# Kernel optimization log

Measured on AMD Instinct MI355X. Metric: run time of the kernel, lower is better.

The kernel has to match this reference:

```python
import jax, jax.numpy as jnp
import numpy as np

F_NHID = 64
C_NHID = 64
U_INIT = F_NHID + C_NHID + 1   # 129
U_OUT = F_NHID + C_NHID        # 128
U_HID = 128
N_AGG = 4
M_INIT = 3 * N_AGG * U_OUT + C_NHID  # 1600
M_HID = 256
M_OUT = C_NHID


def setup_inputs() -> dict:
    key = jax.random.key(0)
    ks = jax.random.split(key, 12)
    B, Nc, Nf = 4, 512, 256
    h_fac = jax.random.normal(ks[0], (B, Nf, F_NHID), dtype=jnp.float32)
    h_cus = jax.random.normal(ks[1], (B, Nc, C_NHID), dtype=jnp.float32)
    edge = jax.random.normal(ks[2], (B, Nc, Nf, 1), dtype=jnp.float32)
    adj = jax.random.randint(ks[3], (B, Nc, Nf), 0, 2).astype(jnp.float32)
    def lin(k, i, o):
        return jax.random.normal(k, (i, o), dtype=jnp.float32) / np.sqrt(i)
    return {
        'h_fac': h_fac, 'h_cus': h_cus, 'edge': edge, 'adj': adj,
        'U_W1': lin(ks[4], U_INIT, U_HID), 'U_b1': jnp.zeros((U_HID,), jnp.float32),
        'U_W2': lin(ks[5], U_HID, U_OUT), 'U_b2': jnp.zeros((U_OUT,), jnp.float32),
        'M_W1': lin(ks[6], M_INIT, M_HID), 'M_b1': jnp.zeros((M_HID,), jnp.float32),
        'M_W2': lin(ks[7], M_HID, M_OUT), 'M_b2': jnp.zeros((M_OUT,), jnp.float32),
    }


def reference(h_fac, h_cus, edge, adj, U_W1, U_b1, U_W2, U_b2, M_W1, M_b1, M_W2, M_b2):
    B, Nc, c = h_cus.shape
    Nf = h_fac.shape[1]
    # Per-edge message input: [customer_feat, facility_feat, edge_scalar] -> (B,Nc,Nf,U_INIT)
    msg = jnp.concatenate([
        jnp.broadcast_to(h_cus[:, :, None, :], (B, Nc, Nf, c)),
        jnp.broadcast_to(h_fac[:, None, :, :], (B, Nc, Nf, h_fac.shape[-1])),
        edge,
    ], axis=-1)
    # U MLP (pretransformation): relu -> linear
    m = jax.nn.relu(msg @ U_W1 + U_b1)
    m = m @ U_W2 + U_b2  # (B, Nc, Nf, U_OUT)

    mask = adj > 0                              # (B, Nc, Nf)
    maskf = mask[..., None].astype(m.dtype)     # (B, Nc, Nf, 1)
    cnt = jnp.sum(maskf, axis=2)                # (B, Nc, 1)
    mean = jnp.sum(m * maskf, axis=2) / cnt     # nanmean over masked entries
    var = jnp.sum(((m - mean[:, :, None, :]) ** 2) * maskf, axis=2) / cnt
    std = jnp.sqrt(var)                         # population std (divides by count)
    mx = jnp.max(jnp.where(mask[..., None], m, -jnp.inf), axis=2)
    mn = jnp.min(jnp.where(mask[..., None], m, jnp.inf), axis=2)

    # Degree-based scalers (get_avgd + scale_amplification/attenuation)
    deg_c = jnp.sum(adj, axis=-1)               # (B, Nc)
    deg_f = jnp.sum(adj, axis=-2)               # (B, Nf)
    avg_d = jnp.mean(jnp.concatenate([jnp.log(deg_c + 1.0), jnp.log(deg_f + 1.0)], axis=-1), axis=-1)  # (B,)
    scale = (jnp.log(deg_c + 1.0) / avg_d[:, None])[..., None]          # (B, Nc, 1)
    scale_inv = jnp.where(scale != 0, 1.0 / scale, jnp.zeros_like(scale))

    feats = [h_cus]
    for a in (mean, std, mx, mn):
        feats.extend([a, a * scale, a * scale_inv])
    h = jnp.concatenate(feats, axis=-1)         # (B, Nc, M_INIT)

    # M MLP (posttransformation): relu -> linear (last activation 'none')
    h = jax.nn.relu(h @ M_W1 + M_b1)
    out = h @ M_W2 + M_b2                       # (B, Nc, C_NHID)
    return out
```

## Files before the change

kernel.cpp:

```cpp
#include <hip/hip_runtime.h>
#include <hip/hip_bf16.h>


using bs8 = __attribute__((ext_vector_type(8))) short;
using f4  = __attribute__((ext_vector_type(4))) float;

__device__ __forceinline__ unsigned short f2bf(float f) {
    union { float f; unsigned int u; } x; x.f = f;
    unsigned int u = x.u + 0x7FFFu + ((x.u >> 16) & 1u);
    return (unsigned short)(u >> 16);
}

__device__ __forceinline__ unsigned int pkbf(float a, float b) {
    __hip_bfloat162 h = __float22bfloat162_rn(make_float2(a, b));
    union { __hip_bfloat162 h; unsigned int u; } c; c.h = h;
    return c.u;
}

__global__ void PNALayer_35081292874189_kernel() {}

#define OFF_AC     0u
#define OFF_AF     1048576u
#define OFF_DEGC   1572864u
#define OFF_DEGF   1581056u
#define OFF_SCALE  1585152u
#define OFF_SINV   1593344u
#define OFF_FEATB  1601536u
#define OFF_HMID   8155392u
#define OFF_W2T    10252544u
#define OFF_W1TB   10318080u
#define WS_NEED    11170048u

__global__ void PNALayer_ws_fail(float* out, int n) {
    int i = blockIdx.x * 256 + threadIdx.x;
    if (i < n) out[i] = 2500.0f;
}

__global__ void PNALayer_prep1(
    const float* h_fac, const float* h_cus, const float* adj,
    const float* U_W1, const float* U_b1, const float* U_W2, const float* M_W1,
    float* wsAc, float* wsAf, float* wsDegC, float* wsDegF,
    unsigned short* wsW2Tb, unsigned short* wsW1Tb)
{
    __shared__ float sH[64];
    __shared__ float sRed[256];
    __shared__ float sT[64][65];
    int bid = blockIdx.x, t = threadIdx.x;

    if (bid < 1024) {
        int b = bid >> 8, f = bid & 255;
        if (t < 64) sH[t] = h_fac[(b * 256 + f) * 64 + t];
        __syncthreads();
        if (t < 128) {
            float acc = 0.f;
            for (int k = 0; k < 64; ++k)
                acc += sH[k] * U_W1[(64 + k) * 128 + t];
            wsAf[(b * 256 + f) * 128 + t] = acc;
        }
        float v = adj[(b * 512 + t) * 256 + f] + adj[(b * 512 + t + 256) * 256 + f];
        sRed[t] = v; __syncthreads();
        for (int s = 128; s > 0; s >>= 1) { if (t < s) sRed[t] += sRed[t + s]; __syncthreads(); }
        if (t == 0) wsDegF[b * 256 + f] = sRed[0];
    } else if (bid < 3072) {
        int bc = bid - 1024;
        if (t < 64) sH[t] = h_cus[bc * 64 + t];
        __syncthreads();
        if (t < 128) {
            float acc = U_b1[t];
            for (int k = 0; k < 64; ++k)
                acc += sH[k] * U_W1[k * 128 + t];
            wsAc[bc * 128 + t] = acc;
        }
        float v = adj[bc * 256 + t];
        sRed[t] = v; __syncthreads();
        for (int s = 128; s > 0; s >>= 1) { if (t < s) sRed[t] += sRed[t + s]; __syncthreads(); }
        if (t == 0) wsDegC[bc] = sRed[0];
    } else if (bid < 3076) {
        int l = bid - 3072;
        int k0 = (l >> 1) * 64, n0 = (l & 1) * 64;
        for (int rep = 0; rep < 16; ++rep) {
            int idx = rep * 256 + t; int r = idx >> 6, c = idx & 63;
            sT[r][c] = U_W2[(k0 + r) * 128 + n0 + c];
        }
        __syncthreads();
        for (int rep = 0; rep < 16; ++rep) {
            int idx = rep * 256 + t; int r = idx >> 6, c = idx & 63;
            wsW2Tb[(n0 + r) * 128 + k0 + c] = f2bf(sT[c][r]);
        }
    } else if (bid < 3176) {
        int l = bid - 3076;
        int k0 = (l % 25) * 64, n0 = (l / 25) * 64;
        for (int rep = 0; rep < 16; ++rep) {
            int idx = rep * 256 + t; int r = idx >> 6, c = idx & 63;
            sT[r][c] = M_W1[(k0 + r) * 256 + n0 + c];
        }
        __syncthreads();
        for (int rep = 0; rep < 16; ++rep) {
            int idx = rep * 256 + t; int r = idx >> 6, c = idx & 63;
            wsW1Tb[(n0 + r) * 1664 + k0 + c] = f2bf(sT[c][r]);
        }
    } else {
        for (int i = 0; i < 64; ++i) {
            int idx = i * 256 + t;
            int n = idx >> 6, k = 1600 + (idx & 63);
            wsW1Tb[n * 1664 + k] = 0;
        }
    }
}

__global__ void PNALayer_prep2(
    const float* wsDegC, const float* wsDegF, float* wsScale, float* wsSinv)
{
    __shared__ float sRed[256];
    __shared__ float sAvg;
    int b = blockIdx.x, t = threadIdx.x;
    float v = logf(wsDegC[b * 512 + t] + 1.f) + logf(wsDegC[b * 512 + t + 256] + 1.f)
            + logf(wsDegF[b * 256 + t] + 1.f);
    sRed[t] = v; __syncthreads();
    for (int s = 128; s > 0; s >>= 1) { if (t < s) sRed[t] += sRed[t + s]; __syncthreads(); }
    if (t == 0) sAvg = sRed[0] / 768.f;
    __syncthreads();
    float avg = sAvg;
    for (int c = t; c < 512; c += 256) {
        float lg = logf(wsDegC[b * 512 + c] + 1.f);
        float sc = lg / avg;
        float si = (sc != 0.f) ? 1.f / sc : 0.f;
        wsScale[b * 512 + c] = sc;
        wsSinv[b * 512 + c] = si;
    }
}

__global__ __launch_bounds__(256, 4) void PNALayer_edge(
    const float* h_cus, const float* edge, const float* adj,
    const float* U_W1, const float* U_b2,
    const float* wsAc, const float* wsAf, const unsigned short* wsW2Tb,
    const float* wsDegC, const float* wsScale, const float* wsSinv,
    unsigned short* featB)
{
    __shared__ __align__(16) unsigned short sM1[64 * 136];
    __shared__ float sE[256];
    __shared__ float sMk[256];
    __shared__ float sAc[128];
    __shared__ float sWe[128];

    int bc = blockIdx.x;
    int b  = bc >> 9;
    int t  = threadIdx.x;
    int w = t >> 6, quad = (t >> 4) & 3, ln = t & 15;

    int r0 = (w * 2 + 0) * 16 + ln;
    int r1 = (w * 2 + 1) * 16 + ln;
    bs8 bw0[4], bw1[4];
#pragma unroll
    for (int kk = 0; kk < 4; ++kk) {
        bw0[kk] = *(const bs8*)(wsW2Tb + r0 * 128 + kk * 32 + quad * 8);
        bw1[kk] = *(const bs8*)(wsW2Tb + r1 * 128 + kk * 32 + quad * 8);
    }
    float b2v0 = U_b2[r0], b2v1 = U_b2[r1];

    sE[t]  = edge[bc * 256 + t];
    sMk[t] = (adj[bc * 256 + t] > 0.f) ? 1.f : 0.f;
    if (t < 128) {
        sAc[t] = wsAc[bc * 128 + t];
        sWe[t] = U_W1[128 * 128 + t];
    }
    if (t < 64) featB[bc * 1600 + t] = f2bf(h_cus[bc * 64 + t]);
    __syncthreads();

    float aS[2]  = {0.f, 0.f},     aQ[2]  = {0.f, 0.f};
    float aMx[2] = {-1e30f, -1e30f}, aMn[2] = {1e30f, 1e30f};

    for (int ft = 0; ft < 4; ++ft) {
#pragma unroll
        for (int i = 0; i < 8; ++i) {
            int idx = i * 256 + t;
            int fl = idx >> 5, k = (idx & 31) * 4;
            int f = ft * 64 + fl;
            float4 af  = *(const float4*)(wsAf + (b * 256 + f) * 128 + k);
            float4 ac4 = *(const float4*)(sAc + k);
            float4 we4 = *(const float4*)(sWe + k);
            float e = sE[f];
            float m0 = fmaxf(ac4.x + af.x + e * we4.x, 0.f);
            float m1 = fmaxf(ac4.y + af.y + e * we4.y, 0.f);
            float m2 = fmaxf(ac4.z + af.z + e * we4.z, 0.f);
            float m3 = fmaxf(ac4.w + af.w + e * we4.w, 0.f);
            uint2 p;
            p.x = pkbf(m0, m1);
            p.y = pkbf(m2, m3);
            *(uint2*)(sM1 + fl * 136 + k) = p;
        }
        __syncthreads();

        f4 acc[4][2];
#pragma unroll
        for (int rt = 0; rt < 4; ++rt) {
            acc[rt][0] = (f4){0.f, 0.f, 0.f, 0.f};
            acc[rt][1] = (f4){0.f, 0.f, 0.f, 0.f};
        }
#pragma unroll
        for (int kk = 0; kk < 4; ++kk) {
            int ko = kk * 32 + quad * 8;
#pragma unroll
            for (int rt = 0; rt < 4; ++rt) {
                bs8 a = *(const bs8*)(sM1 + (rt * 16 + ln) * 136 + ko);
                acc[rt][0] = __builtin_amdgcn_mfma_f32_16x16x32_bf16(a, bw0[kk], acc[rt][0], 0, 0, 0);
                acc[rt][1] = __builtin_amdgcn_mfma_f32_16x16x32_bf16(a, bw1[kk], acc[rt][1], 0, 0, 0);
            }
        }

#pragma unroll
        for (int rt = 0; rt < 4; ++rt) {
#pragma unroll
            for (int i = 0; i < 4; ++i) {
                int f = ft * 64 + rt * 16 + quad * 4 + i;
                if (sMk[f] > 0.f) {
                    float v0 = acc[rt][0][i] + b2v0;
                    float v1 = acc[rt][1][i] + b2v1;
                    aS[0] += v0; aQ[0] += v0 * v0;
                    aMx[0] = fmaxf(aMx[0], v0); aMn[0] = fminf(aMn[0], v0);
                    aS[1] += v1; aQ[1] += v1 * v1;
                    aMx[1] = fmaxf(aMx[1], v1); aMn[1] = fminf(aMn[1], v1);
                }
            }
        }
        __syncthreads();
    }

#pragma unroll
    for (int nt = 0; nt < 2; ++nt) {
        aS[nt]  += __shfl_xor(aS[nt], 16, 64);  aS[nt]  += __shfl_xor(aS[nt], 32, 64);
        aQ[nt]  += __shfl_xor(aQ[nt], 16, 64);  aQ[nt]  += __shfl_xor(aQ[nt], 32, 64);
        aMx[nt] = fmaxf(aMx[nt], __shfl_xor(aMx[nt], 16, 64));
        aMx[nt] = fmaxf(aMx[nt], __shfl_xor(aMx[nt], 32, 64));
        aMn[nt] = fminf(aMn[nt], __shfl_xor(aMn[nt], 16, 64));
        aMn[nt] = fminf(aMn[nt], __shfl_xor(aMn[nt], 32, 64));
    }

    if (quad == 0) {
        float cnt = wsDegC[bc];
        float sc = wsScale[bc], si = wsSinv[bc];
        unsigned short* fr = featB + bc * 1600;
#pragma unroll
        for (int nt = 0; nt < 2; ++nt) {
            int col = (w * 2 + nt) * 16 + ln;
            float mean = aS[nt] / cnt;
            float var  = fmaxf(aQ[nt] / cnt - mean * mean, 0.f);
            float stdv = sqrtf(var);
            float mx = aMx[nt], mn = aMn[nt];
            fr[64 + col]   = f2bf(mean); fr[192 + col]  = f2bf(mean * sc); fr[320 + col]  = f2bf(mean * si);
            fr[448 + col]  = f2bf(stdv); fr[576 + col]  = f2bf(stdv * sc); fr[704 + col]  = f2bf(stdv * si);
            fr[832 + col]  = f2bf(mx);   fr[960 + col]  = f2bf(mx * sc);   fr[1088 + col] = f2bf(mx * si);
            fr[1216 + col] = f2bf(mn);   fr[1344 + col] = f2bf(mn * sc);   fr[1472 + col] = f2bf(mn * si);
        }
    }
}

__global__ __launch_bounds__(256) void PNALayer_mlp1(
    const unsigned short* featB, const unsigned short* wsW1Tb, const float* M_b1,
    float* h_mid)
{
    __shared__ __align__(16) unsigned short sA[16 * 136];
    __shared__ __align__(16) unsigned short sB[64 * 136];
    int t = threadIdx.x;
    int rb = (blockIdx.x >> 2) * 16, cb = (blockIdx.x & 3) * 64;
    int w = t >> 6, quad = (t >> 4) & 3, ln = t & 15;

    f4 acc = (f4){0.f, 0.f, 0.f, 0.f};

    for (int kt = 0; kt < 13; ++kt) {
        int kb = kt * 128;
        {
            int row = t >> 4, c8 = (t & 15) * 8;
            *(uint4*)(sA + row * 136 + c8) =
                *(const uint4*)(featB + (rb + row) * 1600 + kb + c8);
        }
        for (int i = 0; i < 4; ++i) {
            int vi = i * 256 + t;
            int row = vi >> 4, c8 = (vi & 15) * 8;
            *(uint4*)(sB + row * 136 + c8) =
                *(const uint4*)(wsW1Tb + (cb + row) * 1664 + kb + c8);
        }
        __syncthreads();
        for (int kk = 0; kk < 4; ++kk) {
            int ko = kk * 32 + quad * 8;
            bs8 a = *(const bs8*)(sA + ln * 136 + ko);
            bs8 bb = *(const bs8*)(sB + (w * 16 + ln) * 136 + ko);
            acc = __builtin_amdgcn_mfma_f32_16x16x32_bf16(a, bb, acc, 0, 0, 0);
        }
        __syncthreads();
    }
    int col = cb + w * 16 + ln;
    float b1v = M_b1[col];
    for (int i = 0; i < 4; ++i) {
        int row = rb + quad * 4 + i;
        h_mid[row * 256 + col] = fmaxf(acc[i] + b1v, 0.f);
    }
}

__global__ void PNALayer_mlp2(
    const float* h_mid, const float* M_W2, const float* M_b2, float* out)
{
    int idx = blockIdx.x * 256 + threadIdx.x;
    int row = idx >> 6, j = idx & 63;
    float acc = M_b2[j];
    const float* hr = h_mid + row * 256;
    for (int k = 0; k < 256; ++k)
        acc += hr[k] * M_W2[k * 64 + j];
    out[idx] = acc;
}

extern "C" void kernel_launch(void* const* d_in, const int* in_sizes, int n_in,
                              void* d_out, int out_size, void* d_ws, size_t ws_size,
                              hipStream_t stream) {
    const float* h_fac = (const float*)d_in[0];
    const float* h_cus = (const float*)d_in[1];
    const float* edge  = (const float*)d_in[2];
    const float* adj   = (const float*)d_in[3];
    const float* U_W1  = (const float*)d_in[4];
    const float* U_b1  = (const float*)d_in[5];
    const float* U_W2  = (const float*)d_in[6];
    const float* U_b2  = (const float*)d_in[7];
    const float* M_W1  = (const float*)d_in[8];
    const float* M_b1  = (const float*)d_in[9];
    const float* M_W2  = (const float*)d_in[10];
    const float* M_b2  = (const float*)d_in[11];
    (void)in_sizes; (void)n_in;

    float* outp = (float*)d_out;
    int nblk_out = (out_size + 255) / 256;

    if (ws_size < (size_t)WS_NEED) {
        PNALayer_ws_fail<<<nblk_out, 256, 0, stream>>>(outp, out_size);
        return;
    }

    char* ws = (char*)d_ws;
    float*          wsAc   = (float*)(ws + OFF_AC);
    float*          wsAf   = (float*)(ws + OFF_AF);
    float*          wsDegC = (float*)(ws + OFF_DEGC);
    float*          wsDegF = (float*)(ws + OFF_DEGF);
    float*          wsScal = (float*)(ws + OFF_SCALE);
    float*          wsSinv = (float*)(ws + OFF_SINV);
    unsigned short* wsFeatB= (unsigned short*)(ws + OFF_FEATB);
    float*          wsHmid = (float*)(ws + OFF_HMID);
    unsigned short* wsW2Tb = (unsigned short*)(ws + OFF_W2T);
    unsigned short* wsW1Tb = (unsigned short*)(ws + OFF_W1TB);

    PNALayer_prep1<<<3177, 256, 0, stream>>>(
        h_fac, h_cus, adj, U_W1, U_b1, U_W2, M_W1,
        wsAc, wsAf, wsDegC, wsDegF, wsW2Tb, wsW1Tb);
    PNALayer_prep2<<<4, 256, 0, stream>>>(wsDegC, wsDegF, wsScal, wsSinv);
    PNALayer_edge<<<2048, 256, 0, stream>>>(
        h_cus, edge, adj, U_W1, U_b2,
        wsAc, wsAf, wsW2Tb, wsDegC, wsScal, wsSinv, wsFeatB);
    PNALayer_mlp1<<<512, 256, 0, stream>>>(wsFeatB, wsW1Tb, M_b1, wsHmid);
    PNALayer_mlp2<<<512, 256, 0, stream>>>(wsHmid, M_W2, M_b2, outp);
}
```

Measured before the change: 153.0 us.

## Widen edge kernel to 512 threads, hoist bias out of stats, retile mlp1

The edge kernel now runs 512 threads per block. Each wave owns one 16-column output tile instead of two, which halves the per-thread accumulators and register pressure. The U_b2 bias is added after reduction to mean/max/min rather than per element, the elementwise prep uses packed float2 FMA/max, and mlp1 now computes 64-row tiles per block with 4 MFMA accumulators, reusing each B fragment across rows. mlp1 also launches a quarter as many blocks, which raises operand reuse but lowers parallelism.

```diff
diff --git a/kernel.cpp b/kernel.cpp
--- a/kernel.cpp
+++ b/kernel.cpp
@@ -4,6 +4,7 @@
 
 using bs8 = __attribute__((ext_vector_type(8))) short;
 using f4  = __attribute__((ext_vector_type(4))) float;
+using f2  = __attribute__((ext_vector_type(2))) float;
 
 __device__ __forceinline__ unsigned short f2bf(float f) {
     union { float f; unsigned int u; } x; x.f = f;
@@ -130,7 +131,7 @@
     }
 }
 
-__global__ __launch_bounds__(256, 4) void PNALayer_edge(
+__global__ __launch_bounds__(512, 6) void PNALayer_edge(
     const float* h_cus, const float* edge, const float* adj,
     const float* U_W1, const float* U_b2,
     const float* wsAc, const float* wsAf, const unsigned short* wsW2Tb,
@@ -148,63 +149,66 @@
     int t  = threadIdx.x;
     int w = t >> 6, quad = (t >> 4) & 3, ln = t & 15;
 
-    int r0 = (w * 2 + 0) * 16 + ln;
-    int r1 = (w * 2 + 1) * 16 + ln;
-    bs8 bw0[4], bw1[4];
-#pragma unroll
-    for (int kk = 0; kk < 4; ++kk) {
-        bw0[kk] = *(const bs8*)(wsW2Tb + r0 * 128 + kk * 32 + quad * 8);
-        bw1[kk] = *(const bs8*)(wsW2Tb + r1 * 128 + kk * 32 + quad * 8);
-    }
-    float b2v0 = U_b2[r0], b2v1 = U_b2[r1];
-
-    sE[t]  = edge[bc * 256 + t];
-    sMk[t] = (adj[bc * 256 + t] > 0.f) ? 1.f : 0.f;
+    int r0 = w * 16 + ln;
+    bs8 bw[4];
+#pragma unroll
+    for (int kk = 0; kk < 4; ++kk)
+        bw[kk] = *(const bs8*)(wsW2Tb + r0 * 128 + kk * 32 + quad * 8);
+    float b2v = U_b2[r0];
+
+    if (t < 256) {
+        sE[t]  = edge[bc * 256 + t];
+        sMk[t] = (adj[bc * 256 + t] > 0.f) ? 1.f : 0.f;
+    }
     if (t < 128) {
         sAc[t] = wsAc[bc * 128 + t];
         sWe[t] = U_W1[128 * 128 + t];
     }
-    if (t < 64) featB[bc * 1600 + t] = f2bf(h_cus[bc * 64 + t]);
+    if (t >= 128 && t < 192) {
+        int j = t - 128;
+        featB[bc * 1600 + j] = f2bf(h_cus[bc * 64 + j]);
+    }
     __syncthreads();
 
-    float aS[2]  = {0.f, 0.f},     aQ[2]  = {0.f, 0.f};
-    float aMx[2] = {-1e30f, -1e30f}, aMn[2] = {1e30f, 1e30f};
+    float aS = 0.f, aQ = 0.f, aMx = -1e30f, aMn = 1e30f;
+    const f2 zero2 = (f2){0.f, 0.f};
 
     for (int ft = 0; ft < 4; ++ft) {
 #pragma unroll
-        for (int i = 0; i < 8; ++i) {
-            int idx = i * 256 + t;
+        for (int i = 0; i < 4; ++i) {
+            int idx = i * 512 + t;
             int fl = idx >> 5, k = (idx & 31) * 4;
             int f = ft * 64 + fl;
             float4 af  = *(const float4*)(wsAf + (b * 256 + f) * 128 + k);
-            float4 ac4 = *(const float4*)(sAc + k);
-            float4 we4 = *(const float4*)(sWe + k);
+            f2 ac01 = *(const f2*)(sAc + k);
+            f2 ac23 = *(const f2*)(sAc + k + 2);
+            f2 we01 = *(const f2*)(sWe + k);
+            f2 we23 = *(const f2*)(sWe + k + 2);
             float e = sE[f];
-            float m0 = fmaxf(ac4.x + af.x + e * we4.x, 0.f);
-            float m1 = fmaxf(ac4.y + af.y + e * we4.y, 0.f);
-            float m2 = fmaxf(ac4.z + af.z + e * we4.z, 0.f);
-            float m3 = fmaxf(ac4.w + af.w + e * we4.w, 0.f);
+            f2 e2 = (f2){e, e};
+            f2 s01 = ac01 + (f2){af.x, af.y};
+            f2 s23 = ac23 + (f2){af.z, af.w};
+            s01 = __builtin_elementwise_fma(e2, we01, s01);
+            s23 = __builtin_elementwise_fma(e2, we23, s23);
+            f2 r01 = __builtin_elementwise_max(s01, zero2);
+            f2 r23 = __builtin_elementwise_max(s23, zero2);
             uint2 p;
-            p.x = pkbf(m0, m1);
-            p.y = pkbf(m2, m3);
+            p.x = pkbf(r01.x, r01.y);
+            p.y = pkbf(r23.x, r23.y);
             *(uint2*)(sM1 + fl * 136 + k) = p;
         }
         __syncthreads();
 
-        f4 acc[4][2];
-#pragma unroll
-        for (int rt = 0; rt < 4; ++rt) {
-            acc[rt][0] = (f4){0.f, 0.f, 0.f, 0.f};
-            acc[rt][1] = (f4){0.f, 0.f, 0.f, 0.f};
-        }
+        f4 acc[4];
+#pragma unroll
+        for (int rt = 0; rt < 4; ++rt) acc[rt] = (f4){0.f, 0.f, 0.f, 0.f};
 #pragma unroll
         for (int kk = 0; kk < 4; ++kk) {
             int ko = kk * 32 + quad * 8;
 #pragma unroll
             for (int rt = 0; rt < 4; ++rt) {
                 bs8 a = *(const bs8*)(sM1 + (rt * 16 + ln) * 136 + ko);
-                acc[rt][0] = __builtin_amdgcn_mfma_f32_16x16x32_bf16(a, bw0[kk], acc[rt][0], 0, 0, 0);
-                acc[rt][1] = __builtin_amdgcn_mfma_f32_16x16x32_bf16(a, bw1[kk], acc[rt][1], 0, 0, 0);
+                acc[rt] = __builtin_amdgcn_mfma_f32_16x16x32_bf16(a, bw[kk], acc[rt], 0, 0, 0);
             }
         }
 
@@ -214,44 +218,38 @@
             for (int i = 0; i < 4; ++i) {
                 int f = ft * 64 + rt * 16 + quad * 4 + i;
                 if (sMk[f] > 0.f) {
-                    float v0 = acc[rt][0][i] + b2v0;
-                    float v1 = acc[rt][1][i] + b2v1;
-                    aS[0] += v0; aQ[0] += v0 * v0;
-                    aMx[0] = fmaxf(aMx[0], v0); aMn[0] = fminf(aMn[0], v0);
-                    aS[1] += v1; aQ[1] += v1 * v1;
-                    aMx[1] = fmaxf(aMx[1], v1); aMn[1] = fminf(aMn[1], v1);
+                    float v = acc[rt][i];
+                    aS += v;
+                    aQ = fmaf(v, v, aQ);
+                    aMx = fmaxf(aMx, v);
+                    aMn = fminf(aMn, v);
                 }
             }
         }
         __syncthreads();
     }
 
-#pragma unroll
-    for (int nt = 0; nt < 2; ++nt) {
-        aS[nt]  += __shfl_xor(aS[nt], 16, 64);  aS[nt]  += __shfl_xor(aS[nt], 32, 64);
-        aQ[nt]  += __shfl_xor(aQ[nt], 16, 64);  aQ[nt]  += __shfl_xor(aQ[nt], 32, 64);
-        aMx[nt] = fmaxf(aMx[nt], __shfl_xor(aMx[nt], 16, 64));
-        aMx[nt] = fmaxf(aMx[nt], __shfl_xor(aMx[nt], 32, 64));
-        aMn[nt] = fminf(aMn[nt], __shfl_xor(aMn[nt], 16, 64));
-        aMn[nt] = fminf(aMn[nt], __shfl_xor(aMn[nt], 32, 64));
-    }
+    aS  += __shfl_xor(aS, 16, 64);  aS  += __shfl_xor(aS, 32, 64);
+    aQ  += __shfl_xor(aQ, 16, 64);  aQ  += __shfl_xor(aQ, 32, 64);
+    aMx = fmaxf(aMx, __shfl_xor(aMx, 16, 64));
+    aMx = fmaxf(aMx, __shfl_xor(aMx, 32, 64));
+    aMn = fminf(aMn, __shfl_xor(aMn, 16, 64));
+    aMn = fminf(aMn, __shfl_xor(aMn, 32, 64));
 
     if (quad == 0) {
         float cnt = wsDegC[bc];
         float sc = wsScale[bc], si = wsSinv[bc];
         unsigned short* fr = featB + bc * 1600;
-#pragma unroll
-        for (int nt = 0; nt < 2; ++nt) {
-            int col = (w * 2 + nt) * 16 + ln;
-            float mean = aS[nt] / cnt;
-            float var  = fmaxf(aQ[nt] / cnt - mean * mean, 0.f);
-            float stdv = sqrtf(var);
-            float mx = aMx[nt], mn = aMn[nt];
-            fr[64 + col]   = f2bf(mean); fr[192 + col]  = f2bf(mean * sc); fr[320 + col]  = f2bf(mean * si);
-            fr[448 + col]  = f2bf(stdv); fr[576 + col]  = f2bf(stdv * sc); fr[704 + col]  = f2bf(stdv * si);
-            fr[832 + col]  = f2bf(mx);   fr[960 + col]  = f2bf(mx * sc);   fr[1088 + col] = f2bf(mx * si);
-            fr[1216 + col] = f2bf(mn);   fr[1344 + col] = f2bf(mn * sc);   fr[1472 + col] = f2bf(mn * si);
-        }
+        int col = w * 16 + ln;
+        float meanr = aS / cnt;
+        float mean  = meanr + b2v;
+        float var   = fmaxf(aQ / cnt - meanr * meanr, 0.f);
+        float stdv  = sqrtf(var);
+        float mx = aMx + b2v, mn = aMn + b2v;
+        fr[64 + col]   = f2bf(mean); fr[192 + col]  = f2bf(mean * sc); fr[320 + col]  = f2bf(mean * si);
+        fr[448 + col]  = f2bf(stdv); fr[576 + col]  = f2bf(stdv * sc); fr[704 + col]  = f2bf(stdv * si);
+        fr[832 + col]  = f2bf(mx);   fr[960 + col]  = f2bf(mx * sc);   fr[1088 + col] = f2bf(mx * si);
+        fr[1216 + col] = f2bf(mn);   fr[1344 + col] = f2bf(mn * sc);   fr[1472 + col] = f2bf(mn * si);
     }
 }
 
@@ -259,21 +257,26 @@
     const unsigned short* featB, const unsigned short* wsW1Tb, const float* M_b1,
     float* h_mid)
 {
-    __shared__ __align__(16) unsigned short sA[16 * 136];
+    __shared__ __align__(16) unsigned short sA[64 * 136];
     __shared__ __align__(16) unsigned short sB[64 * 136];
     int t = threadIdx.x;
-    int rb = (blockIdx.x >> 2) * 16, cb = (blockIdx.x & 3) * 64;
+    int rb = (blockIdx.x >> 2) * 64, cb = (blockIdx.x & 3) * 64;
     int w = t >> 6, quad = (t >> 4) & 3, ln = t & 15;
 
-    f4 acc = (f4){0.f, 0.f, 0.f, 0.f};
+    f4 acc[4];
+#pragma unroll
+    for (int rt = 0; rt < 4; ++rt) acc[rt] = (f4){0.f, 0.f, 0.f, 0.f};
 
     for (int kt = 0; kt < 13; ++kt) {
         int kb = kt * 128;
-        {
-            int row = t >> 4, c8 = (t & 15) * 8;
+#pragma unroll
+        for (int i = 0; i < 4; ++i) {
+            int vi = i * 256 + t;
+            int row = vi >> 4, c8 = (vi & 15) * 8;
             *(uint4*)(sA + row * 136 + c8) =
                 *(const uint4*)(featB + (rb + row) * 1600 + kb + c8);
         }
+#pragma unroll
         for (int i = 0; i < 4; ++i) {
             int vi = i * 256 + t;
             int row = vi >> 4, c8 = (vi & 15) * 8;
@@ -281,19 +284,27 @@
                 *(const uint4*)(wsW1Tb + (cb + row) * 1664 + kb + c8);
         }
         __syncthreads();
+#pragma unroll
         for (int kk = 0; kk < 4; ++kk) {
             int ko = kk * 32 + quad * 8;
-            bs8 a = *(const bs8*)(sA + ln * 136 + ko);
             bs8 bb = *(const bs8*)(sB + (w * 16 + ln) * 136 + ko);
-            acc = __builtin_amdgcn_mfma_f32_16x16x32_bf16(a, bb, acc, 0, 0, 0);
+#pragma unroll
+            for (int rt = 0; rt < 4; ++rt) {
+                bs8 a = *(const bs8*)(sA + (rt * 16 + ln) * 136 + ko);
+                acc[rt] = __builtin_amdgcn_mfma_f32_16x16x32_bf16(a, bb, acc[rt], 0, 0, 0);
+            }
         }
         __syncthreads();
     }
     int col = cb + w * 16 + ln;
     float b1v = M_b1[col];
-    for (int i = 0; i < 4; ++i) {
-        int row = rb + quad * 4 + i;
-        h_mid[row * 256 + col] = fmaxf(acc[i] + b1v, 0.f);
+#pragma unroll
+    for (int rt = 0; rt < 4; ++rt) {
+#pragma unroll
+        for (int i = 0; i < 4; ++i) {
+            int row = rb + rt * 16 + quad * 4 + i;
+            h_mid[row * 256 + col] = fmaxf(acc[rt][i] + b1v, 0.f);
+        }
     }
 }
 
@@ -304,6 +315,7 @@
     int row = idx >> 6, j = idx & 63;
     float acc = M_b2[j];
     const float* hr = h_mid + row * 256;
+#pragma unroll 8
     for (int k = 0; k < 256; ++k)
         acc += hr[k] * M_W2[k * 64 + j];
     out[idx] = acc;
@@ -350,9 +362,9 @@
         h_fac, h_cus, adj, U_W1, U_b1, U_W2, M_W1,
         wsAc, wsAf, wsDegC, wsDegF, wsW2Tb, wsW1Tb);
     PNALayer_prep2<<<4, 256, 0, stream>>>(wsDegC, wsDegF, wsScal, wsSinv);
-    PNALayer_edge<<<2048, 256, 0, stream>>>(
+    PNALayer_edge<<<2048, 512, 0, stream>>>(
         h_cus, edge, adj, U_W1, U_b2,
         wsAc, wsAf, wsW2Tb, wsDegC, wsScal, wsSinv, wsFeatB);
-    PNALayer_mlp1<<<512, 256, 0, stream>>>(wsFeatB, wsW1Tb, M_b1, wsHmid);
+    PNALayer_mlp1<<<128, 256, 0, stream>>>(wsFeatB, wsW1Tb, M_b1, wsHmid);
     PNALayer_mlp2<<<512, 256, 0, stream>>>(wsHmid, M_W2, M_b2, outp);
 }
```

Measured after the change: 159.9 us. +4.5%, slower.
